# Kernel optimization log

Hardware: AMD Instinct MI355X
Metric: run time of the kernel (lower is better)

The kernel has to match this reference:

```python
import jax, jax.numpy as jnp
import numpy as np

D = 1024
H = 8          # MHA fallback num_heads
DH = D // H
DFF = 4096     # mlp_ratio * hidden_size
EPS = 1e-6


def _ln(x, g, b):
    mu = jnp.mean(x, axis=-1, keepdims=True)
    var = jnp.mean((x - mu) ** 2, axis=-1, keepdims=True)
    return (x - mu) * jax.lax.rsqrt(var + EPS) * g + b


def setup_inputs() -> dict:
    key = jax.random.key(0)
    ks = jax.random.split(key, 16)
    s = 0.02
    return {
        "x": jax.random.normal(ks[0], (8, 1024, D), jnp.float32),
        "c": jax.random.normal(ks[1], (8, D), jnp.float32),
        # Mamba-block (attention fallback) params
        "m_ada_w": jax.random.normal(ks[2], (D, 3 * D), jnp.float32) * s,
        "m_ada_b": jnp.zeros((3 * D,), jnp.float32),
        "m_norm_g": jnp.ones((D,), jnp.float32),
        "m_norm_b": jnp.zeros((D,), jnp.float32),
        "in_proj_w": jax.random.normal(ks[3], (3 * D, D), jnp.float32) * s,
        "in_proj_b": jnp.zeros((3 * D,), jnp.float32),
        "out_proj_w": jax.random.normal(ks[4], (D, D), jnp.float32) * s,
        "out_proj_b": jnp.zeros((D,), jnp.float32),
        # FeedForward-block params
        "f_ada_w": jax.random.normal(ks[5], (D, 3 * D), jnp.float32) * s,
        "f_ada_b": jnp.zeros((3 * D,), jnp.float32),
        "f_norm_g": jnp.ones((D,), jnp.float32),
        "f_norm_b": jnp.zeros((D,), jnp.float32),
        "w1": jax.random.normal(ks[6], (D, DFF), jnp.float32) * s,
        "b1": jnp.zeros((DFF,), jnp.float32),
        "w2": jax.random.normal(ks[7], (DFF, D), jnp.float32) * s,
        "b2": jnp.zeros((D,), jnp.float32),
    }


def reference(x, c, m_ada_w, m_ada_b, m_norm_g, m_norm_b, in_proj_w, in_proj_b,
              out_proj_w, out_proj_b, f_ada_w, f_ada_b, f_norm_g, f_norm_b,
              w1, b1, w2, b2):
    B, N, _ = x.shape
    # ---- MambaBlock (MHA fallback), dropout = identity (eval) ----
    mod = jax.nn.silu(c) @ m_ada_w + m_ada_b              # (B, 3D)
    shift, scale, gate = jnp.split(mod, 3, axis=-1)
    h = _ln(x, m_norm_g, m_norm_b)
    h = h * (1.0 + scale[:, None, :]) + shift[:, None, :]
    qkv = h @ in_proj_w.T + in_proj_b                      # (B, N, 3D)
    q, k, v = jnp.split(qkv, 3, axis=-1)
    q = q.reshape(B, N, H, DH)
    k = k.reshape(B, N, H, DH)
    v = v.reshape(B, N, H, DH)
    scores = jnp.einsum("bqhd,bkhd->bhqk", q, k) / np.sqrt(DH).astype(np.float32)
    attn = jax.nn.softmax(scores, axis=-1)
    o = jnp.einsum("bhqk,bkhd->bqhd", attn, v).reshape(B, N, D)
    o = o @ out_proj_w.T + out_proj_b
    x = x + gate[:, None, :] * o
    # ---- FeedForward block ----
    mod2 = jax.nn.silu(c) @ f_ada_w + f_ada_b
    shift2, scale2, gate2 = jnp.split(mod2, 3, axis=-1)
    h = _ln(x, f_norm_g, f_norm_b)
    h = h * (1.0 + scale2[:, None, :]) + shift2[:, None, :]
    h = jax.nn.gelu(h @ w1 + b1, approximate=False) @ w2 + b2
    return x + gate2[:, None, :] * h
```

## Files before the change

kernel.cpp:

```cpp
#include <hip/hip_runtime.h>

typedef __bf16 bf16x8 __attribute__((ext_vector_type(8)));
typedef float f32x4 __attribute__((ext_vector_type(4)));

__device__ __forceinline__ unsigned short f2bf(float f) {
    unsigned int u = __float_as_uint(f);
    unsigned int r = (u + 0x7FFFu + ((u >> 16) & 1u)) >> 16;
    return (unsigned short)r;
}

__device__ __forceinline__ void gload16(const void* g, void* l) {
    __builtin_amdgcn_global_load_lds(
        (const __attribute__((address_space(1))) unsigned int*)g,
        (__attribute__((address_space(3))) unsigned int*)l, 16, 0, 0);
}

__device__ __forceinline__ void barrier_raw() {
    asm volatile("" ::: "memory");
    __builtin_amdgcn_s_barrier();
    asm volatile("" ::: "memory");
}

__device__ __forceinline__ void vmwait0() {
    asm volatile("s_waitcnt vmcnt(0)" ::: "memory");
}

__device__ __forceinline__ float gelu_fast(float u) {
    float z = 1.595769122f * u + 0.071354816f * u * u * u;
    return u / (1.f + __expf(-z));
}

__global__ __launch_bounds__(256) void f2b4(const float* __restrict__ in,
                                            unsigned short* __restrict__ out) {
    size_t i = ((size_t)blockIdx.x * 256 + threadIdx.x) * 4;
    float4 v = *(const float4*)(in + i);
    ushort4 o;
    o.x = f2bf(v.x); o.y = f2bf(v.y); o.z = f2bf(v.z); o.w = f2bf(v.w);
    *(ushort4*)(out + i) = o;
}

__global__ __launch_bounds__(256) void transpose_f2b(const float* __restrict__ in,
                                                     unsigned short* __restrict__ out,
                                                     int R, int C) {
    __shared__ float tile[32][33];
    int r0 = blockIdx.y * 32, c0 = blockIdx.x * 32;
    int tx = threadIdx.x & 31, ty = threadIdx.x >> 5;
#pragma unroll
    for (int i = 0; i < 4; i++) {
        int r = ty + i * 8;
        tile[r][tx] = in[(size_t)(r0 + r) * C + c0 + tx];
    }
    __syncthreads();
#pragma unroll
    for (int i = 0; i < 4; i++) {
        int r = ty + i * 8;
        out[(size_t)(c0 + r) * R + r0 + tx] = f2bf(tile[tx][r]);
    }
}

__global__ __launch_bounds__(256) void transpose_v(const unsigned short* __restrict__ qkv,
                                                   unsigned short* __restrict__ vt) {
    __shared__ unsigned short tile[32][33];
    int head = blockIdx.z;
    int b = head >> 3;
    int n0 = blockIdx.x * 32, d0 = blockIdx.y * 32;
    int tx = threadIdx.x & 31, ty = threadIdx.x >> 5;
    const unsigned short* src = qkv + (size_t)(b * 1024) * 3072 + 2048 + (head & 7) * 128;
#pragma unroll
    for (int i = 0; i < 4; i++) {
        int n = ty + i * 8;
        tile[n][tx] = src[(size_t)(n0 + n) * 3072 + d0 + tx];
    }
    __syncthreads();
#pragma unroll
    for (int i = 0; i < 4; i++) {
        int d = ty + i * 8;
        vt[((size_t)head * 128 + d0 + d) * 1024 + n0 + tx] = tile[tx][d];
    }
}

__global__ __launch_bounds__(256) void ada_mod_part(const float* __restrict__ c,
                                                    const float* __restrict__ W,
                                                    float* __restrict__ partial) {
    __shared__ float sc[8 * 64];
    int kc = blockIdx.y * 64;
    for (int i = threadIdx.x; i < 512; i += 256) {
        int b = i >> 6, k = i & 63;
        float cv = c[b * 1024 + kc + k];
        sc[i] = cv / (1.f + __expf(-cv));
    }
    __syncthreads();
    int j = blockIdx.x * 256 + threadIdx.x;
    float acc[8] = {0, 0, 0, 0, 0, 0, 0, 0};
    for (int k = 0; k < 64; k++) {
        float w = W[(size_t)(kc + k) * 3072 + j];
#pragma unroll
        for (int b = 0; b < 8; b++) acc[b] += sc[b * 64 + k] * w;
    }
#pragma unroll
    for (int b = 0; b < 8; b++) partial[((size_t)blockIdx.y * 8 + b) * 3072 + j] = acc[b];
}

__global__ __launch_bounds__(256) void ada_reduce(const float* __restrict__ partial,
                                                  const float* __restrict__ bias,
                                                  float* __restrict__ out) {
    int idx = blockIdx.x * 256 + threadIdx.x;
    int b = idx / 3072;
    int jj = idx - b * 3072;
    float s = bias[jj];
#pragma unroll
    for (int ch = 0; ch < 16; ch++) s += partial[((size_t)ch * 8 + b) * 3072 + jj];
    out[idx] = s;
}

__global__ __launch_bounds__(256) void ln_mod_kernel(const float* __restrict__ x,
                                                     const float* __restrict__ gamma,
                                                     const float* __restrict__ beta,
                                                     const float* __restrict__ mods,
                                                     unsigned short* __restrict__ out) {
    int row = blockIdx.x;
    int b = row >> 10;
    float4 v = ((const float4*)(x + (size_t)row * 1024))[threadIdx.x];
    float s = v.x + v.y + v.z + v.w;
    float s2 = v.x * v.x + v.y * v.y + v.z * v.z + v.w * v.w;
#pragma unroll
    for (int d = 1; d < 64; d <<= 1) { s += __shfl_xor(s, d); s2 += __shfl_xor(s2, d); }
    __shared__ float red[8];
    int lane = threadIdx.x & 63, wid = threadIdx.x >> 6;
    if (lane == 0) { red[wid] = s; red[4 + wid] = s2; }
    __syncthreads();
    float S = red[0] + red[1] + red[2] + red[3];
    float S2 = red[4] + red[5] + red[6] + red[7];
    float mu = S * (1.f / 1024.f);
    float var = S2 * (1.f / 1024.f) - mu * mu;
    float rs = rsqrtf(var + 1e-6f);
    const float* mrow = mods + b * 3072;
    int j0 = threadIdx.x * 4;
    float hv[4] = {v.x, v.y, v.z, v.w};
    ushort4 o;
    unsigned short* op = (unsigned short*)&o;
#pragma unroll
    for (int i = 0; i < 4; i++) {
        int j = j0 + i;
        float hh = (hv[i] - mu) * rs * gamma[j] + beta[j];
        hh = hh * (1.f + mrow[1024 + j]) + mrow[j];
        op[i] = f2bf(hh);
    }
    *(ushort4*)(out + (size_t)row * 1024 + j0) = o;
}

template <int CMAP, int EP>
__global__ __launch_bounds__(512, 2) void gemmv2(const unsigned short* __restrict__ A,
                                                 const unsigned short* __restrict__ Bt,
                                                 int N, int K,
                                                 const float* __restrict__ bias,
                                                 const float* __restrict__ xres,
                                                 const float* __restrict__ mods,
                                                 float* __restrict__ outf,
                                                 unsigned short* __restrict__ outb) {
    constexpr int AE = 128 * 64;
    constexpr int BE = 256 * 64;
    extern __shared__ __align__(16) char smem[];
    __bf16* As = (__bf16*)smem;
    __bf16* Bs = As + 2 * AE;

    int tid = threadIdx.x, lane = tid & 63, wid = tid >> 6;
    int wr = wid >> 2, wc = wid & 3;
    int t = lane & 15, g = lane >> 4;
    int xk = (t & 7) * 8;

    int xcd = blockIdx.x & 7, s = blockIdx.x >> 3;
    int by, bx;
    if (CMAP == 0) { by = xcd + 8 * (s & 7); bx = s >> 3; }
    else           { bx = xcd & 3; by = (xcd >> 2) * 32 + s; }
    int rowA0 = by * 128, colB0 = bx * 256;

    int rin = tid >> 3, cblk = tid & 7;
    int scol = (cblk ^ (rin & 7)) * 8;

    auto stage = [&](int nb, int kt) {
        int k0 = kt << 6;
#pragma unroll
        for (int sl = 0; sl < 2; sl++)
            gload16(A + (size_t)(rowA0 + sl * 64 + rin) * K + k0 + scol,
                    As + nb * AE + sl * 4096 + tid * 8);
#pragma unroll
        for (int sl = 0; sl < 4; sl++)
            gload16(Bt + (size_t)(colB0 + sl * 64 + rin) * K + k0 + scol,
                    Bs + nb * BE + sl * 4096 + tid * 8);
    };

    f32x4 acc[4][4];
#pragma unroll
    for (int m = 0; m < 4; m++)
#pragma unroll
        for (int n = 0; n < 4; n++) acc[m][n] = (f32x4){0.f, 0.f, 0.f, 0.f};

    stage(0, 0);
    vmwait0();
    barrier_raw();

    int NT = K >> 6;
#pragma unroll 1
    for (int kt = 0; kt < NT; ++kt) {
        const __bf16* Ac = As + (kt & 1) * AE;
        const __bf16* Bc = Bs + (kt & 1) * BE;
        bool more = (kt + 1) < NT;
        if (more) stage((kt & 1) ^ 1, kt + 1);

#pragma unroll
        for (int ks = 0; ks < 2; ks++) {
            bf16x8 a[4], b[4];
#pragma unroll
            for (int m = 0; m < 4; m++)
                a[m] = *(const bf16x8*)&Ac[(wr * 64 + m * 16 + t) * 64 + ((ks * 32 + g * 8) ^ xk)];
#pragma unroll
            for (int n = 0; n < 4; n++)
                b[n] = *(const bf16x8*)&Bc[(wc * 64 + n * 16 + t) * 64 + ((ks * 32 + g * 8) ^ xk)];
            __builtin_amdgcn_s_setprio(1);
#pragma unroll
            for (int m = 0; m < 4; m++)
#pragma unroll
                for (int n = 0; n < 4; n++)
                    acc[m][n] = __builtin_amdgcn_mfma_f32_16x16x32_bf16(a[m], b[n], acc[m][n], 0, 0, 0);
            __builtin_amdgcn_s_setprio(0);
        }

        if (more) {
            vmwait0();
            barrier_raw();
        }
    }

    int row0 = rowA0 + wr * 64, col0 = colB0 + wc * 64;
#pragma unroll
    for (int m = 0; m < 4; m++)
#pragma unroll
        for (int n = 0; n < 4; n++) {
            int col = col0 + n * 16 + t;
#pragma unroll
            for (int r = 0; r < 4; r++) {
                int row = row0 + m * 16 + g * 4 + r;
                float v = acc[m][n][r];
                if (EP == 0) {
                    outb[(size_t)row * N + col] = f2bf(v + bias[col]);
                } else if (EP == 1) {
                    int bb = row >> 10;
                    float gt = mods[bb * 3072 + 2048 + col];
                    outf[(size_t)row * 1024 + col] =
                        xres[(size_t)row * 1024 + col] + gt * (v + bias[col]);
                } else if (EP == 2) {
                    outb[(size_t)row * N + col] = f2bf(gelu_fast(v + bias[col]));
                } else {
                    int bb = row >> 10;
                    float gt = mods[bb * 3072 + 2048 + col];
                    outf[(size_t)row * 1024 + col] += gt * (v + bias[col]);
                }
            }
        }
}

__global__ __launch_bounds__(512, 4) void attn_kernel(const unsigned short* __restrict__ qkv,
                                                      const unsigned short* __restrict__ vt,
                                                      unsigned short* __restrict__ o) {
    extern __shared__ __align__(16) char asmem[];
    __bf16* Ks = (__bf16*)asmem;
    __bf16* Vts = Ks + 2 * 64 * 128;

    int bid = blockIdx.x;
    int logical = (bid & 7) * 64 + (bid >> 3);
    int q0 = (logical & 7) * 128;
    int bh = logical >> 3;
    int b = bh >> 3, h = bh & 7;
    int tid = threadIdx.x, lane = tid & 63, w = tid >> 6;
    int t = lane & 15, g = lane >> 4;
    int swzt = (t & 7) << 4;

    const unsigned short* qbase = qkv + (size_t)(b * 1024) * 3072 + h * 128;
    int qrow = q0 + w * 16 + t;
    bf16x8 qf[4];
#pragma unroll
    for (int ks = 0; ks < 4; ks++)
        qf[ks] = *(const bf16x8*)(qbase + (size_t)qrow * 3072 + ks * 32 + g * 8);

    f32x4 Oa[8];
#pragma unroll
    for (int n = 0; n < 8; n++) Oa[n] = (f32x4){0.f, 0.f, 0.f, 0.f};
    float m_r = -1e30f, l_r = 0.f;
    const float scale = 0.08838834764831845f;

    int krow = tid >> 4;
    int ksrc = (((tid & 15) * 16) ^ ((krow & 7) << 4)) >> 1;
    int vrow = tid >> 3;
    int vsrc = (((tid & 7) * 16) ^ ((vrow & 7) << 4)) >> 1;
    const unsigned short* vtg = vt + (size_t)bh * 128 * 1024;

    auto stage = [&](int buf, int kv0) {
        const unsigned short* kb = qkv + (size_t)(b * 1024 + kv0) * 3072 + 1024 + h * 128;
#pragma unroll
        for (int cc = 0; cc < 2; cc++) {
            gload16(kb + (size_t)(cc * 32 + krow) * 3072 + ksrc,
                    (void*)(Ks + buf * 8192 + cc * 4096 + tid * 8));
            gload16(vtg + (size_t)(cc * 64 + vrow) * 1024 + kv0 + vsrc,
                    (void*)(Vts + buf * 8192 + cc * 4096 + tid * 8));
        }
    };

    stage(0, 0);
    vmwait0();
    barrier_raw();

#pragma unroll 1
    for (int tile = 0; tile < 16; ++tile) {
        int cur = tile & 1;
        bool more = tile < 15;
        if (more) stage(cur ^ 1, (tile + 1) * 64);
        const __bf16* Kc = Ks + cur * 8192;
        const __bf16* Vc = Vts + cur * 8192;

        f32x4 St[4];
#pragma unroll
        for (int n = 0; n < 4; n++) St[n] = (f32x4){0.f, 0.f, 0.f, 0.f};
        __builtin_amdgcn_s_setprio(1);
#pragma unroll
        for (int ks = 0; ks < 4; ks++) {
#pragma unroll
            for (int n = 0; n < 4; n++) {
                bf16x8 kf = *(const bf16x8*)&Kc[(n * 16 + t) * 128 + (((ks * 64 + g * 16) ^ swzt) >> 1)];
                St[n] = __builtin_amdgcn_mfma_f32_16x16x32_bf16(kf, qf[ks], St[n], 0, 0, 0);
            }
        }
        __builtin_amdgcn_s_setprio(0);

        float mx = -1e30f;
#pragma unroll
        for (int n = 0; n < 4; n++)
#pragma unroll
            for (int r = 0; r < 4; r++) mx = fmaxf(mx, St[n][r]);
        mx *= scale;
        mx = fmaxf(mx, __shfl_xor(mx, 16));
        mx = fmaxf(mx, __shfl_xor(mx, 32));
        float mn = fmaxf(m_r, mx);
        float alpha = __expf(m_r - mn);
        m_r = mn;
        float p[4][4];
        float rs = 0.f;
#pragma unroll
        for (int n = 0; n < 4; n++)
#pragma unroll
            for (int r = 0; r < 4; r++) {
                float pv = __expf(St[n][r] * scale - mn);
                p[n][r] = pv;
                rs += pv;
            }
        rs += __shfl_xor(rs, 16);
        rs += __shfl_xor(rs, 32);
        l_r = l_r * alpha + rs;

        unsigned P01[4], P23[4];
#pragma unroll
        for (int n = 0; n < 4; n++) {
            P01[n] = (unsigned)f2bf(p[n][0]) | ((unsigned)f2bf(p[n][1]) << 16);
            P23[n] = (unsigned)f2bf(p[n][2]) | ((unsigned)f2bf(p[n][3]) << 16);
        }

#pragma unroll
        for (int r = 0; r < 4; r++) {
            float ar = __shfl(alpha, (lane & 48) + g * 4 + r);
#pragma unroll
            for (int n2 = 0; n2 < 8; n2++) Oa[n2][r] *= ar;
        }

#pragma unroll
        for (int ks2 = 0; ks2 < 2; ks2++) {
            int e = ks2 * 2, od = ks2 * 2 + 1;
            unsigned s16a = (g < 2) ? P01[e] : P01[od];
            unsigned s16b = (g < 2) ? P23[e] : P23[od];
            unsigned s32a = (g & 1) ? P01[e] : P01[od];
            unsigned s32b = (g & 1) ? P23[e] : P23[od];
            unsigned s48a = (g >= 2) ? P01[e] : P01[od];
            unsigned s48b = (g >= 2) ? P23[e] : P23[od];
            unsigned r16a = __shfl_xor(s16a, 16), r16b = __shfl_xor(s16b, 16);
            unsigned r32a = __shfl_xor(s32a, 32), r32b = __shfl_xor(s32b, 32);
            unsigned r48a = __shfl_xor(s48a, 48), r48b = __shfl_xor(s48b, 48);
            union { unsigned u[4]; bf16x8 v; } pa;
            pa.u[0] = (g == 0) ? P01[e] : (g == 1) ? r48a : (g == 2) ? r32a : r16a;
            pa.u[1] = (g == 0) ? P23[e] : (g == 1) ? r48b : (g == 2) ? r32b : r16b;
            pa.u[2] = (g == 0) ? r16a : (g == 1) ? r32a : (g == 2) ? r48a : P01[od];
            pa.u[3] = (g == 0) ? r16b : (g == 1) ? r32b : (g == 2) ? r48b : P23[od];
            __builtin_amdgcn_s_setprio(1);
#pragma unroll
            for (int n2 = 0; n2 < 8; n2++) {
                bf16x8 vf = *(const bf16x8*)&Vc[(n2 * 16 + t) * 64 + (((ks2 * 64 + g * 16) ^ swzt) >> 1)];
                Oa[n2] = __builtin_amdgcn_mfma_f32_16x16x32_bf16(pa.v, vf, Oa[n2], 0, 0, 0);
            }
            __builtin_amdgcn_s_setprio(0);
        }

        if (more) {
            vmwait0();
            barrier_raw();
        }
    }

#pragma unroll
    for (int r = 0; r < 4; r++) {
        float lq = __shfl(l_r, (lane & 48) + g * 4 + r);
        float inv = 1.f / lq;
        int orow = q0 + w * 16 + g * 4 + r;
#pragma unroll
        for (int n2 = 0; n2 < 8; n2++)
            o[(size_t)(b * 1024 + orow) * 1024 + h * 128 + n2 * 16 + t] = f2bf(Oa[n2][r] * inv);
    }
}

extern "C" void kernel_launch(void* const* d_in, const int* in_sizes, int n_in,
                              void* d_out, int out_size, void* d_ws, size_t ws_size,
                              hipStream_t stream) {
    const float* x          = (const float*)d_in[0];
    const float* c          = (const float*)d_in[1];
    const float* m_ada_w    = (const float*)d_in[2];
    const float* m_ada_b    = (const float*)d_in[3];
    const float* m_norm_g   = (const float*)d_in[4];
    const float* m_norm_b   = (const float*)d_in[5];
    const float* in_proj_w  = (const float*)d_in[6];
    const float* in_proj_b  = (const float*)d_in[7];
    const float* out_proj_w = (const float*)d_in[8];
    const float* out_proj_b = (const float*)d_in[9];
    const float* f_ada_w    = (const float*)d_in[10];
    const float* f_ada_b    = (const float*)d_in[11];
    const float* f_norm_g   = (const float*)d_in[12];
    const float* f_norm_b   = (const float*)d_in[13];
    const float* w1         = (const float*)d_in[14];
    const float* b1         = (const float*)d_in[15];
    const float* w2         = (const float*)d_in[16];
    const float* b2         = (const float*)d_in[17];
    float* out = (float*)d_out;
    char* ws = (char*)d_ws;

    unsigned short* Wq   = (unsigned short*)(ws + 0);
    unsigned short* Wo   = (unsigned short*)(ws + 6291456);
    unsigned short* vt   = (unsigned short*)(ws + 8388608);
    unsigned short* W1t  = (unsigned short*)(ws + 8388608);
    unsigned short* W2t  = (unsigned short*)(ws + 16777216);
    float*          modm = (float*)(ws + 25165824);
    float*          modf = (float*)(ws + 25264128);
    unsigned short* hbuf = (unsigned short*)(ws + 25362432);
    float*          part = (float*)(ws + 25362432);
    float*          part2= (float*)(ws + 25362432 + 2097152);
    unsigned short* qkv  = (unsigned short*)(ws + 42139648);
    unsigned short* obuf = (unsigned short*)(ws + 92471296);
    unsigned short* h2   = (unsigned short*)(ws + 42139648);

    hipFuncSetAttribute((const void*)&gemmv2<0, 0>, hipFuncAttributeMaxDynamicSharedMemorySize, 98304);
    hipFuncSetAttribute((const void*)&gemmv2<0, 2>, hipFuncAttributeMaxDynamicSharedMemorySize, 98304);
    hipFuncSetAttribute((const void*)&gemmv2<0, 1>, hipFuncAttributeMaxDynamicSharedMemorySize, 98304);
    hipFuncSetAttribute((const void*)&gemmv2<1, 3>, hipFuncAttributeMaxDynamicSharedMemorySize, 98304);
    hipFuncSetAttribute((const void*)&attn_kernel, hipFuncAttributeMaxDynamicSharedMemorySize, 65536);

    hipLaunchKernelGGL(ada_mod_part, dim3(12, 16), dim3(256), 0, stream, c, m_ada_w, part);
    hipLaunchKernelGGL(ada_mod_part, dim3(12, 16), dim3(256), 0, stream, c, f_ada_w, part2);
    hipLaunchKernelGGL(ada_reduce, dim3(96), dim3(256), 0, stream, part, m_ada_b, modm);
    hipLaunchKernelGGL(ada_reduce, dim3(96), dim3(256), 0, stream, part2, f_ada_b, modf);

    hipLaunchKernelGGL(f2b4, dim3(3072), dim3(256), 0, stream, in_proj_w, Wq);
    hipLaunchKernelGGL(f2b4, dim3(1024), dim3(256), 0, stream, out_proj_w, Wo);

    hipLaunchKernelGGL(ln_mod_kernel, dim3(8192), dim3(256), 0, stream, x, m_norm_g, m_norm_b, modm, hbuf);
    hipLaunchKernelGGL(HIP_KERNEL_NAME(gemmv2<0, 0>), dim3(768), dim3(512), 98304, stream,
                       hbuf, Wq, 3072, 1024, in_proj_b, (const float*)nullptr,
                       (const float*)nullptr, (float*)nullptr, qkv);
    hipLaunchKernelGGL(transpose_v, dim3(32, 4, 64), dim3(256), 0, stream, qkv, vt);
    hipLaunchKernelGGL(attn_kernel, dim3(512), dim3(512), 65536, stream, qkv, vt, obuf);
    hipLaunchKernelGGL(HIP_KERNEL_NAME(gemmv2<0, 1>), dim3(256), dim3(512), 98304, stream,
                       obuf, Wo, 1024, 1024, out_proj_b, x, modm, out, (unsigned short*)nullptr);

    hipLaunchKernelGGL(transpose_f2b, dim3(128, 32), dim3(256), 0, stream, w1, W1t, 1024, 4096);
    hipLaunchKernelGGL(transpose_f2b, dim3(32, 128), dim3(256), 0, stream, w2, W2t, 4096, 1024);

    hipLaunchKernelGGL(ln_mod_kernel, dim3(8192), dim3(256), 0, stream, out, f_norm_g, f_norm_b, modf, hbuf);
    hipLaunchKernelGGL(HIP_KERNEL_NAME(gemmv2<0, 2>), dim3(1024), dim3(512), 98304, stream,
                       hbuf, W1t, 4096, 1024, b1, (const float*)nullptr,
                       (const float*)nullptr, (float*)nullptr, h2);
    hipLaunchKernelGGL(HIP_KERNEL_NAME(gemmv2<1, 3>), dim3(256), dim3(512), 98304, stream,
                       h2, W2t, 1024, 4096, b2, (const float*)nullptr, modf, out,
                       (unsigned short*)nullptr);
}
```

Measured before the change: 386.8 us.

## Retile GEMMs to K=32 stages, smaller N-tiles, and fuse V transpose into QKV epilogue

Replaces the GEMM kernel with a variant that stages K in 32-wide slices with a matching LDS swizzle, halving shared memory per block so that 4 blocks fit per CU. The N=1024 GEMMs now use 128x128 tiles with 256 threads to produce more blocks. A generic XCD-chunked tile mapping replaces the hardcoded one. The QKV GEMM epilogue writes V directly in transposed layout, which removes the separate transpose_v kernel and its extra pass over V. Shorter K steps mean more barriers per FLOP, and the transposed stores are 4-element strided writes.

```diff
diff --git a/kernel.cpp b/kernel.cpp
--- a/kernel.cpp
+++ b/kernel.cpp
@@ -55,27 +55,6 @@
     for (int i = 0; i < 4; i++) {
         int r = ty + i * 8;
         out[(size_t)(c0 + r) * R + r0 + tx] = f2bf(tile[tx][r]);
-    }
-}
-
-__global__ __launch_bounds__(256) void transpose_v(const unsigned short* __restrict__ qkv,
-                                                   unsigned short* __restrict__ vt) {
-    __shared__ unsigned short tile[32][33];
-    int head = blockIdx.z;
-    int b = head >> 3;
-    int n0 = blockIdx.x * 32, d0 = blockIdx.y * 32;
-    int tx = threadIdx.x & 31, ty = threadIdx.x >> 5;
-    const unsigned short* src = qkv + (size_t)(b * 1024) * 3072 + 2048 + (head & 7) * 128;
-#pragma unroll
-    for (int i = 0; i < 4; i++) {
-        int n = ty + i * 8;
-        tile[n][tx] = src[(size_t)(n0 + n) * 3072 + d0 + tx];
-    }
-    __syncthreads();
-#pragma unroll
-    for (int i = 0; i < 4; i++) {
-        int d = ty + i * 8;
-        vt[((size_t)head * 128 + d0 + d) * 1024 + n0 + tx] = tile[tx][d];
     }
 }
 
@@ -149,45 +128,52 @@
     *(ushort4*)(out + (size_t)row * 1024 + j0) = o;
 }
 
-template <int CMAP, int EP>
-__global__ __launch_bounds__(512, 2) void gemmv2(const unsigned short* __restrict__ A,
-                                                 const unsigned short* __restrict__ Bt,
-                                                 int N, int K,
-                                                 const float* __restrict__ bias,
-                                                 const float* __restrict__ xres,
-                                                 const float* __restrict__ mods,
-                                                 float* __restrict__ outf,
-                                                 unsigned short* __restrict__ outb) {
-    constexpr int AE = 128 * 64;
-    constexpr int BE = 256 * 64;
+template <int NF, int EP>
+__global__ __launch_bounds__(NF * 128, 4) void gemmo(const unsigned short* __restrict__ A,
+                                                     const unsigned short* __restrict__ Bt,
+                                                     int N, int K, int nx,
+                                                     const float* __restrict__ bias,
+                                                     const float* __restrict__ xres,
+                                                     const float* __restrict__ mods,
+                                                     float* __restrict__ outf,
+                                                     unsigned short* __restrict__ outb,
+                                                     unsigned short* __restrict__ vt) {
+    constexpr int AE = 128 * 32;
+    constexpr int BE = NF * 64 * 32;
     extern __shared__ __align__(16) char smem[];
     __bf16* As = (__bf16*)smem;
     __bf16* Bs = As + 2 * AE;
 
     int tid = threadIdx.x, lane = tid & 63, wid = tid >> 6;
-    int wr = wid >> 2, wc = wid & 3;
+    int wr, wc;
+    if (NF == 4) { wr = wid >> 2; wc = wid & 3; }
+    else         { wr = wid >> 1; wc = wid & 1; }
     int t = lane & 15, g = lane >> 4;
-    int xk = (t & 7) * 8;
-
-    int xcd = blockIdx.x & 7, s = blockIdx.x >> 3;
-    int by, bx;
-    if (CMAP == 0) { by = xcd + 8 * (s & 7); bx = s >> 3; }
-    else           { bx = xcd & 3; by = (xcd >> 2) * 32 + s; }
-    int rowA0 = by * 128, colB0 = bx * 256;
-
-    int rin = tid >> 3, cblk = tid & 7;
-    int scol = (cblk ^ (rin & 7)) * 8;
+    int xk2 = ((t >> 1) & 3) * 8;
+
+    int nwg = gridDim.x, chunk = nwg >> 3;
+    int swz = (blockIdx.x & 7) * chunk + (blockIdx.x >> 3);
+    int bx = swz % nx, by = swz / nx;
+    int rowA0 = by * 128, colB0 = bx * (NF * 64);
+
+    int rin = tid >> 2, cblk = tid & 3;
+    int scol = (cblk ^ ((rin >> 1) & 3)) * 8;
 
     auto stage = [&](int nb, int kt) {
-        int k0 = kt << 6;
-#pragma unroll
-        for (int sl = 0; sl < 2; sl++)
-            gload16(A + (size_t)(rowA0 + sl * 64 + rin) * K + k0 + scol,
-                    As + nb * AE + sl * 4096 + tid * 8);
-#pragma unroll
-        for (int sl = 0; sl < 4; sl++)
-            gload16(Bt + (size_t)(colB0 + sl * 64 + rin) * K + k0 + scol,
-                    Bs + nb * BE + sl * 4096 + tid * 8);
+        int k0 = kt << 5;
+        if (NF == 4) {
+            gload16(A + (size_t)(rowA0 + rin) * K + k0 + scol, As + nb * AE + tid * 8);
+            gload16(Bt + (size_t)(colB0 + rin) * K + k0 + scol, Bs + nb * BE + tid * 8);
+            gload16(Bt + (size_t)(colB0 + 128 + rin) * K + k0 + scol,
+                    Bs + nb * BE + 4096 + tid * 8);
+        } else {
+            gload16(A + (size_t)(rowA0 + rin) * K + k0 + scol, As + nb * AE + tid * 8);
+            gload16(A + (size_t)(rowA0 + 64 + rin) * K + k0 + scol,
+                    As + nb * AE + 2048 + tid * 8);
+            gload16(Bt + (size_t)(colB0 + rin) * K + k0 + scol, Bs + nb * BE + tid * 8);
+            gload16(Bt + (size_t)(colB0 + 64 + rin) * K + k0 + scol,
+                    Bs + nb * BE + 2048 + tid * 8);
+        }
     };
 
     f32x4 acc[4][4];
@@ -200,31 +186,29 @@
     vmwait0();
     barrier_raw();
 
-    int NT = K >> 6;
-#pragma unroll 1
+    int NT = K >> 5;
+#pragma unroll 2
     for (int kt = 0; kt < NT; ++kt) {
         const __bf16* Ac = As + (kt & 1) * AE;
         const __bf16* Bc = Bs + (kt & 1) * BE;
         bool more = (kt + 1) < NT;
         if (more) stage((kt & 1) ^ 1, kt + 1);
 
-#pragma unroll
-        for (int ks = 0; ks < 2; ks++) {
-            bf16x8 a[4], b[4];
-#pragma unroll
-            for (int m = 0; m < 4; m++)
-                a[m] = *(const bf16x8*)&Ac[(wr * 64 + m * 16 + t) * 64 + ((ks * 32 + g * 8) ^ xk)];
+        bf16x8 a[4], b[4];
+#pragma unroll
+        for (int m = 0; m < 4; m++)
+            a[m] = *(const bf16x8*)&Ac[(wr * 64 + m * 16 + t) * 32 + ((g * 8) ^ xk2)];
+#pragma unroll
+        for (int n = 0; n < 4; n++)
+            b[n] = *(const bf16x8*)&Bc[(wc * 64 + n * 16 + t) * 32 + ((g * 8) ^ xk2)];
+
+        __builtin_amdgcn_s_setprio(1);
+#pragma unroll
+        for (int m = 0; m < 4; m++)
 #pragma unroll
             for (int n = 0; n < 4; n++)
-                b[n] = *(const bf16x8*)&Bc[(wc * 64 + n * 16 + t) * 64 + ((ks * 32 + g * 8) ^ xk)];
-            __builtin_amdgcn_s_setprio(1);
-#pragma unroll
-            for (int m = 0; m < 4; m++)
-#pragma unroll
-                for (int n = 0; n < 4; n++)
-                    acc[m][n] = __builtin_amdgcn_mfma_f32_16x16x32_bf16(a[m], b[n], acc[m][n], 0, 0, 0);
-            __builtin_amdgcn_s_setprio(0);
-        }
+                acc[m][n] = __builtin_amdgcn_mfma_f32_16x16x32_bf16(a[m], b[n], acc[m][n], 0, 0, 0);
+        __builtin_amdgcn_s_setprio(0);
 
         if (more) {
             vmwait0();
@@ -233,28 +217,43 @@
     }
 
     int row0 = rowA0 + wr * 64, col0 = colB0 + wc * 64;
+    bool vpart = (EP == 0) && (colB0 >= 2048);
 #pragma unroll
     for (int m = 0; m < 4; m++)
 #pragma unroll
         for (int n = 0; n < 4; n++) {
             int col = col0 + n * 16 + t;
-#pragma unroll
-            for (int r = 0; r < 4; r++) {
-                int row = row0 + m * 16 + g * 4 + r;
-                float v = acc[m][n][r];
-                if (EP == 0) {
-                    outb[(size_t)row * N + col] = f2bf(v + bias[col]);
-                } else if (EP == 1) {
-                    int bb = row >> 10;
-                    float gt = mods[bb * 3072 + 2048 + col];
-                    outf[(size_t)row * 1024 + col] =
-                        xres[(size_t)row * 1024 + col] + gt * (v + bias[col]);
-                } else if (EP == 2) {
-                    outb[(size_t)row * N + col] = f2bf(gelu_fast(v + bias[col]));
-                } else {
-                    int bb = row >> 10;
-                    float gt = mods[bb * 3072 + 2048 + col];
-                    outf[(size_t)row * 1024 + col] += gt * (v + bias[col]);
+            if (EP == 0 && vpart) {
+                int hcol = col - 2048;
+                int hh = hcol >> 7, d = hcol & 127;
+                int bb = row0 >> 10;
+                int ntok = (row0 + m * 16 + g * 4) & 1023;
+                float bs = bias[col];
+                ushort4 vv;
+                vv.x = f2bf(acc[m][n][0] + bs);
+                vv.y = f2bf(acc[m][n][1] + bs);
+                vv.z = f2bf(acc[m][n][2] + bs);
+                vv.w = f2bf(acc[m][n][3] + bs);
+                *(ushort4*)(vt + (((size_t)(bb * 8 + hh) * 128 + d) * 1024 + ntok)) = vv;
+            } else {
+#pragma unroll
+                for (int r = 0; r < 4; r++) {
+                    int row = row0 + m * 16 + g * 4 + r;
+                    float v = acc[m][n][r];
+                    if (EP == 0) {
+                        outb[(size_t)row * N + col] = f2bf(v + bias[col]);
+                    } else if (EP == 1) {
+                        int bb = row >> 10;
+                        float gt = mods[bb * 3072 + 2048 + col];
+                        outf[(size_t)row * 1024 + col] =
+                            xres[(size_t)row * 1024 + col] + gt * (v + bias[col]);
+                    } else if (EP == 2) {
+                        outb[(size_t)row * N + col] = f2bf(gelu_fast(v + bias[col]));
+                    } else {
+                        int bb = row >> 10;
+                        float gt = mods[bb * 3072 + 2048 + col];
+                        outf[(size_t)row * 1024 + col] += gt * (v + bias[col]);
+                    }
                 }
             }
         }
@@ -452,10 +451,10 @@
     unsigned short* obuf = (unsigned short*)(ws + 92471296);
     unsigned short* h2   = (unsigned short*)(ws + 42139648);
 
-    hipFuncSetAttribute((const void*)&gemmv2<0, 0>, hipFuncAttributeMaxDynamicSharedMemorySize, 98304);
-    hipFuncSetAttribute((const void*)&gemmv2<0, 2>, hipFuncAttributeMaxDynamicSharedMemorySize, 98304);
-    hipFuncSetAttribute((const void*)&gemmv2<0, 1>, hipFuncAttributeMaxDynamicSharedMemorySize, 98304);
-    hipFuncSetAttribute((const void*)&gemmv2<1, 3>, hipFuncAttributeMaxDynamicSharedMemorySize, 98304);
+    hipFuncSetAttribute((const void*)&gemmo<4, 0>, hipFuncAttributeMaxDynamicSharedMemorySize, 49152);
+    hipFuncSetAttribute((const void*)&gemmo<4, 2>, hipFuncAttributeMaxDynamicSharedMemorySize, 49152);
+    hipFuncSetAttribute((const void*)&gemmo<2, 1>, hipFuncAttributeMaxDynamicSharedMemorySize, 32768);
+    hipFuncSetAttribute((const void*)&gemmo<2, 3>, hipFuncAttributeMaxDynamicSharedMemorySize, 32768);
     hipFuncSetAttribute((const void*)&attn_kernel, hipFuncAttributeMaxDynamicSharedMemorySize, 65536);
 
     hipLaunchKernelGGL(ada_mod_part, dim3(12, 16), dim3(256), 0, stream, c, m_ada_w, part);
@@ -467,22 +466,22 @@
     hipLaunchKernelGGL(f2b4, dim3(1024), dim3(256), 0, stream, out_proj_w, Wo);
 
     hipLaunchKernelGGL(ln_mod_kernel, dim3(8192), dim3(256), 0, stream, x, m_norm_g, m_norm_b, modm, hbuf);
-    hipLaunchKernelGGL(HIP_KERNEL_NAME(gemmv2<0, 0>), dim3(768), dim3(512), 98304, stream,
-                       hbuf, Wq, 3072, 1024, in_proj_b, (const float*)nullptr,
-                       (const float*)nullptr, (float*)nullptr, qkv);
-    hipLaunchKernelGGL(transpose_v, dim3(32, 4, 64), dim3(256), 0, stream, qkv, vt);
+    hipLaunchKernelGGL(HIP_KERNEL_NAME(gemmo<4, 0>), dim3(768), dim3(512), 49152, stream,
+                       hbuf, Wq, 3072, 1024, 12, in_proj_b, (const float*)nullptr,
+                       (const float*)nullptr, (float*)nullptr, qkv, vt);
     hipLaunchKernelGGL(attn_kernel, dim3(512), dim3(512), 65536, stream, qkv, vt, obuf);
-    hipLaunchKernelGGL(HIP_KERNEL_NAME(gemmv2<0, 1>), dim3(256), dim3(512), 98304, stream,
-                       obuf, Wo, 1024, 1024, out_proj_b, x, modm, out, (unsigned short*)nullptr);
+    hipLaunchKernelGGL(HIP_KERNEL_NAME(gemmo<2, 1>), dim3(512), dim3(256), 32768, stream,
+                       obuf, Wo, 1024, 1024, 8, out_proj_b, x, modm, out,
+                       (unsigned short*)nullptr, (unsigned short*)nullptr);
 
     hipLaunchKernelGGL(transpose_f2b, dim3(128, 32), dim3(256), 0, stream, w1, W1t, 1024, 4096);
     hipLaunchKernelGGL(transpose_f2b, dim3(32, 128), dim3(256), 0, stream, w2, W2t, 4096, 1024);
 
     hipLaunchKernelGGL(ln_mod_kernel, dim3(8192), dim3(256), 0, stream, out, f_norm_g, f_norm_b, modf, hbuf);
-    hipLaunchKernelGGL(HIP_KERNEL_NAME(gemmv2<0, 2>), dim3(1024), dim3(512), 98304, stream,
-                       hbuf, W1t, 4096, 1024, b1, (const float*)nullptr,
-                       (const float*)nullptr, (float*)nullptr, h2);
-    hipLaunchKernelGGL(HIP_KERNEL_NAME(gemmv2<1, 3>), dim3(256), dim3(512), 98304, stream,
-                       h2, W2t, 1024, 4096, b2, (const float*)nullptr, modf, out,
-                       (unsigned short*)nullptr);
-}
+    hipLaunchKernelGGL(HIP_KERNEL_NAME(gemmo<4, 2>), dim3(1024), dim3(512), 49152, stream,
+                       hbuf, W1t, 4096, 1024, 16, b1, (const float*)nullptr,
+                       (const float*)nullptr, (float*)nullptr, h2, (unsigned short*)nullptr);
+    hipLaunchKernelGGL(HIP_KERNEL_NAME(gemmo<2, 3>), dim3(512), dim3(256), 32768, stream,
+                       h2, W2t, 1024, 4096, 8, b2, (const float*)nullptr, modf, out,
+                       (unsigned short*)nullptr, (unsigned short*)nullptr);
+}
```

After: 385.8 us. Within noise of the previous version (-0.2%).
